# Kernel tuning notes

Hardware: AMD Instinct MI355X
Metric: run time of the kernel (lower is better)

## Reference

```python
import jax, jax.numpy as jnp
import numpy as np

NUM_HEADS = 8
NUM_LEVELS = 4
NUM_POINTS = 4


def setup_inputs() -> dict:
    key = jax.random.key(0)
    kq, kp, kv, k1, k2, k3, k4 = jax.random.split(key, 7)
    B, Q, C = 4, 4096, 256
    M, L, P = NUM_HEADS, NUM_LEVELS, NUM_POINTS
    shapes_np = np.array([[128, 128], [64, 64], [32, 32], [16, 16]], dtype=np.int32)
    sizes = shapes_np[:, 0] * shapes_np[:, 1]
    N = int(sizes.sum())  # 21760
    level_index = jnp.asarray(np.concatenate([[0], np.cumsum(sizes)[:-1]]).astype(np.int32))
    q = jax.random.normal(kq, (B, Q, C), jnp.float32)
    p = jax.random.uniform(kp, (B, Q, L, 2), jnp.float32)  # normalized ref points
    v = jax.random.normal(kv, (B, N, C), jnp.float32)
    # proj_offset bias: radial grid init from reset_parameters()
    t = np.arange(M, dtype=np.float32) * (2.0 * np.pi / M)
    grid = np.stack([np.cos(t), np.sin(t)], -1)
    grid = grid / np.abs(grid).max(-1, keepdims=True)
    grid = np.tile(grid[:, None, None, :], (1, L, P, 1)) * np.arange(1, P + 1, dtype=np.float32)[None, None, :, None]
    b_off = jnp.asarray(grid.reshape(-1))
    s = 1.0 / np.sqrt(C).astype(np.float32)
    W_off = jax.random.normal(k1, (C, M * L * P * 2), jnp.float32) * 0.01
    W_attn = jax.random.normal(k2, (C, M * L * P), jnp.float32) * s
    b_attn = jnp.zeros((M * L * P,), jnp.float32)
    W_val = jax.random.normal(k3, (C, C), jnp.float32) * s
    b_val = jnp.zeros((C,), jnp.float32)
    W_out = jax.random.normal(k4, (C, C), jnp.float32) * s
    b_out = jnp.zeros((C,), jnp.float32)
    return {"q": q, "p": p, "v": v, "shapes": jnp.asarray(shapes_np), "level_index": level_index,
            "W_off": W_off, "b_off": b_off, "W_attn": W_attn, "b_attn": b_attn,
            "W_val": W_val, "b_val": b_val, "W_out": W_out, "b_out": b_out}


def _ms_deform_attn(q, p, v, shapes, level_index, W_off, b_off, W_attn, b_attn, W_val, b_val, W_out, b_out):
    B, Q, C = q.shape
    M, L, P = NUM_HEADS, NUM_LEVELS, NUM_POINTS
    D = C // M
    N = v.shape[1]
    # value projection -> [B, M, N, D] (head-major for gather)
    v_p = (v @ W_val + b_val).reshape(B, N, M, D).transpose(0, 2, 1, 3)
    # attention weights, softmax over L*P (classic MSDeformAttn kernel contract)
    attn = jax.nn.softmax((q @ W_attn + b_attn).reshape(B, Q, M, L * P), axis=-1)
    attn = attn.reshape(B, Q, M, L, P)
    # sampling locations (P==2 reference-point branch)
    off = (q @ W_off + b_off).reshape(B, Q, M, L, P, 2)
    norm = jnp.stack([shapes[:, 1], shapes[:, 0]], -1).astype(jnp.float32)  # (W, H) per level
    loc = p[:, :, None, :, None, :] + off / norm[None, None, None, :, None, :]  # [B,Q,M,L,P,2]

    out = jnp.zeros((B, M, Q, D), jnp.float32)
    for l in range(L):
        Hf = shapes[l, 0].astype(jnp.float32)
        Wf = shapes[l, 1].astype(jnp.float32)
        Hi = shapes[l, 0]
        Wi = shapes[l, 1]
        base = level_index[l]
        # grid_sample(align_corners=False) convention: pixel = loc*size - 0.5
        x = loc[:, :, :, l, :, 0] * Wf - 0.5  # [B,Q,M,P]
        y = loc[:, :, :, l, :, 1] * Hf - 0.5
        x0 = jnp.floor(x)
        y0 = jnp.floor(y)
        lx, ly = x - x0, y - y0
        x0i = x0.astype(jnp.int32)
        y0i = y0.astype(jnp.int32)

        def corner(xi, yi, w):
            valid = (xi >= 0) & (xi < Wi) & (yi >= 0) & (yi < Hi)
            idx = base + jnp.clip(yi, 0, Hi - 1) * Wi + jnp.clip(xi, 0, Wi - 1)  # [B,Q,M,P]
            idx = idx.transpose(0, 2, 1, 3).reshape(B, M, Q * P)
            g = jnp.take_along_axis(v_p, idx[..., None], axis=2).reshape(B, M, Q, P, D)
            wv = (w * valid.astype(w.dtype)).transpose(0, 2, 1, 3)[..., None]  # [B,M,Q,P,1]
            return g * wv

        samp = (corner(x0i, y0i, (1 - lx) * (1 - ly))
                + corner(x0i + 1, y0i, lx * (1 - ly))
                + corner(x0i, y0i + 1, (1 - lx) * ly)
                + corner(x0i + 1, y0i + 1, lx * ly))  # [B,M,Q,P,D]
        a_l = attn[:, :, :, l, :].transpose(0, 2, 1, 3)  # [B,M,Q,P]
        out = out + jnp.einsum('bmqpd,bmqp->bmqd', samp, a_l)

    out = out.transpose(0, 2, 1, 3).reshape(B, Q, M * D)
    return out @ W_out + b_out


def reference(q, p, v, shapes, level_index, W_off, b_off, W_attn, b_attn, W_val, b_val, W_out, b_out):
    return _ms_deform_attn(q, p, v, shapes, level_index, W_off, b_off, W_attn, b_attn, W_val, b_val, W_out, b_out)
```

## Files before the change

kernel.cpp:

```cpp
#include <hip/hip_runtime.h>
#include <cstddef>

#define BB 4
#define QQ 4096
#define MM 8
#define NN 21760

typedef __bf16 bf16_8 __attribute__((ext_vector_type(8)));
typedef __bf16 bf16_4 __attribute__((ext_vector_type(4)));
typedef float  floatx4 __attribute__((ext_vector_type(4)));

__global__ __launch_bounds__(256) void prep_weights(
    const float* __restrict__ Wv, const float* __restrict__ Wa,
    const float* __restrict__ Wo, const float* __restrict__ Wu,
    const float* __restrict__ ba, const float* __restrict__ bo,
    __bf16* __restrict__ Wt, float* __restrict__ biasq)
{
    const int gid = blockIdx.x * 256 + threadIdx.x;
    if (gid < 65536) {
        const int n = gid >> 8, k = gid & 255;
        Wt[gid] = (__bf16)Wv[k * 256 + n];
    } else if (gid < 163840) {
        const int o = gid - 65536;
        const int n = o >> 8, k = o & 255;
        Wt[gid] = (__bf16)(n < 128 ? Wa[k * 128 + n] : Wo[k * 256 + (n - 128)]);
    } else if (gid < 229376) {
        const int o = gid - 163840;
        const int n = o >> 8, k = o & 255;
        Wt[gid] = (__bf16)Wu[k * 256 + n];
    } else if (gid < 229760) {
        const int j = gid - 229376;
        biasq[j] = (j < 128) ? ba[j] : bo[j - 128];
    }
}

template<typename AT, int NCOLS, int MODE>
__global__ __launch_bounds__(256) void gemm_bd(
    const AT* __restrict__ A,
    const __bf16* __restrict__ Wn,
    const float* __restrict__ bias,
    void* __restrict__ Cout,
    int tokens, int ldc)
{
    constexpr int NJ = NCOLS / 64;
    const int z    = blockIdx.z;
    const int row0 = blockIdx.y * 64;
    const AT* Ab = A + (size_t)z * tokens * 256;

    __shared__ __bf16 As[2][64][68];

    const int tid  = threadIdx.x;
    const int lane = tid & 63;
    const int wave = tid >> 6;
    const int quad = lane >> 4;
    const int l16  = lane & 15;
    const int wave_f = wave * (NCOLS / 4);

    floatx4 acc[NJ][4] = {};

    if (sizeof(AT) == 4) {
        const float* Af = (const float*)Ab;
        #pragma unroll
        for (int c = 0; c < 4; ++c) {
            const int cid = c * 256 + tid;
            const int r   = cid >> 4;
            const int kc  = (cid & 15) * 4;
            const float4 av = *(const float4*)(Af + (size_t)(row0 + r) * 256 + kc);
            bf16_4 w;
            w[0] = (__bf16)av.x; w[1] = (__bf16)av.y; w[2] = (__bf16)av.z; w[3] = (__bf16)av.w;
            *(bf16_4*)&As[0][r][kc] = w;
        }
    } else {
        const __bf16* Ah = (const __bf16*)Ab;
        #pragma unroll
        for (int c = 0; c < 2; ++c) {
            const int cid = c * 256 + tid;
            const int r   = cid >> 3;
            const int kc  = (cid & 7) * 8;
            *(bf16_8*)&As[0][r][kc] = *(const bf16_8*)(Ah + (size_t)(row0 + r) * 256 + kc);
        }
    }
    __syncthreads();

    for (int i = 0; i < 4; ++i) {
        const int k0  = i * 64;
        const int cur = i & 1;

        float4 a4[4]; bf16_8 a8[2];
        if (i < 3) {
            if (sizeof(AT) == 4) {
                const float* Af = (const float*)Ab;
                #pragma unroll
                for (int c = 0; c < 4; ++c) {
                    const int cid = c * 256 + tid;
                    const int r   = cid >> 4;
                    const int kc  = (cid & 15) * 4;
                    a4[c] = *(const float4*)(Af + (size_t)(row0 + r) * 256 + k0 + 64 + kc);
                }
            } else {
                const __bf16* Ah = (const __bf16*)Ab;
                #pragma unroll
                for (int c = 0; c < 2; ++c) {
                    const int cid = c * 256 + tid;
                    const int r   = cid >> 3;
                    const int kc  = (cid & 7) * 8;
                    a8[c] = *(const bf16_8*)(Ah + (size_t)(row0 + r) * 256 + k0 + 64 + kc);
                }
            }
        }

        bf16_8 wf[2][NJ];
        #pragma unroll
        for (int h = 0; h < 2; ++h)
            #pragma unroll
            for (int j = 0; j < NJ; ++j)
                wf[h][j] = *(const bf16_8*)(Wn + (size_t)(wave_f + j * 16 + l16) * 256
                                             + k0 + h * 32 + quad * 8);

        #pragma unroll
        for (int h = 0; h < 2; ++h) {
            bf16_8 af[4];
            #pragma unroll
            for (int it = 0; it < 4; ++it)
                af[it] = *(const bf16_8*)&As[cur][it * 16 + l16][h * 32 + quad * 8];
            #pragma unroll
            for (int j = 0; j < NJ; ++j)
                #pragma unroll
                for (int it = 0; it < 4; ++it)
                    acc[j][it] = __builtin_amdgcn_mfma_f32_16x16x32_bf16(wf[h][j], af[it], acc[j][it], 0, 0, 0);
        }

        if (i < 3) {
            if (sizeof(AT) == 4) {
                #pragma unroll
                for (int c = 0; c < 4; ++c) {
                    const int cid = c * 256 + tid;
                    const int r   = cid >> 4;
                    const int kc  = (cid & 15) * 4;
                    bf16_4 w;
                    w[0] = (__bf16)a4[c].x; w[1] = (__bf16)a4[c].y;
                    w[2] = (__bf16)a4[c].z; w[3] = (__bf16)a4[c].w;
                    *(bf16_4*)&As[cur ^ 1][r][kc] = w;
                }
            } else {
                #pragma unroll
                for (int c = 0; c < 2; ++c) {
                    const int cid = c * 256 + tid;
                    const int r   = cid >> 3;
                    const int kc  = (cid & 7) * 8;
                    *(bf16_8*)&As[cur ^ 1][r][kc] = a8[c];
                }
            }
            __syncthreads();
        }
    }

    #pragma unroll
    for (int j = 0; j < NJ; ++j) {
        const int n0 = wave_f + j * 16 + quad * 4;
        const float4 b4 = *(const float4*)(bias + n0);
        #pragma unroll
        for (int it = 0; it < 4; ++it) {
            const int token = row0 + it * 16 + l16;
            const float v0 = acc[j][it][0] + b4.x;
            const float v1 = acc[j][it][1] + b4.y;
            const float v2 = acc[j][it][2] + b4.z;
            const float v3 = acc[j][it][3] + b4.w;
            if (MODE == 0) {
                float4 o; o.x = v0; o.y = v1; o.z = v2; o.w = v3;
                *(float4*)((float*)Cout + ((size_t)z * tokens + token) * ldc + n0) = o;
            } else {
                const int mh = n0 >> 5, dd = n0 & 31;
                bf16_4 ob;
                ob[0] = (__bf16)v0; ob[1] = (__bf16)v1; ob[2] = (__bf16)v2; ob[3] = (__bf16)v3;
                *(bf16_4*)((__bf16*)Cout + (((size_t)z * 8 + mh) * NN + token) * 32 + dd) = ob;
            }
        }
    }
}

__device__ __forceinline__ float bflo(unsigned u) { return __uint_as_float(u << 16); }
__device__ __forceinline__ float bfhi(unsigned u) { return __uint_as_float(u & 0xffff0000u); }

__global__ __launch_bounds__(512) void sampler(
    const __bf16* __restrict__ vp,
    const float* __restrict__ gqp,
    const float* __restrict__ pref,
    __bf16* __restrict__ mid)
{
    const int t    = threadIdx.x;
    const int m    = t >> 6;
    const int lane = t & 63;
    const int s    = lane >> 2;
    const int c    = lane & 3;
    const int l    = s >> 2;
    const int bq   = blockIdx.x;
    const int b    = bq >> 12;

    const int   Hi = 128 >> l;
    const float Hf = (float)Hi;
    const int   base = (l == 0) ? 0 : (l == 1) ? 16384 : (l == 2) ? 20480 : 21504;

    const float logit = gqp[(size_t)bq * 384 + m * 16 + s];
    const float e = __expf(logit);
    float sum = e;
    #pragma unroll
    for (int k = 4; k < 64; k <<= 1) sum += __shfl_xor(sum, k, 64);
    const float a = e * __builtin_amdgcn_rcpf(sum);

    const float2 off = *(const float2*)(gqp + (size_t)bq * 384 + 128 + (m * 16 + s) * 2);
    const float2 pr  = *(const float2*)(pref + (size_t)bq * 8 + l * 2);

    const float x = fmaf(pr.x, Hf, off.x - 0.5f);
    const float y = fmaf(pr.y, Hf, off.y - 0.5f);
    const float x0f = floorf(x), y0f = floorf(y);
    const float lx = x - x0f, ly = y - y0f;
    const int x0 = (int)x0f, y0 = (int)y0f;
    const int cx0 = min(max(x0, 0), Hi - 1), cx1 = min(max(x0 + 1, 0), Hi - 1);
    const int cy0 = min(max(y0, 0), Hi - 1), cy1 = min(max(y0 + 1, 0), Hi - 1);
    const bool vx0 = (x0 >= 0) && (x0 < Hi), vx1 = (x0 + 1 >= 0) && (x0 + 1 < Hi);
    const bool vy0 = (y0 >= 0) && (y0 < Hi), vy1 = (y0 + 1 >= 0) && (y0 + 1 < Hi);
    const float w00 = a * (1.f - lx) * (1.f - ly) * ((vx0 && vy0) ? 1.f : 0.f);
    const float w10 = a * lx * (1.f - ly) * ((vx1 && vy0) ? 1.f : 0.f);
    const float w01 = a * (1.f - lx) * ly * ((vx0 && vy1) ? 1.f : 0.f);
    const float w11 = a * lx * ly * ((vx1 && vy1) ? 1.f : 0.f);

    const __bf16* vbase = vp + ((size_t)b * 8 + m) * NN * 32;
    const uint4 u00 = *((const uint4*)(vbase + (size_t)(base + cy0 * Hi + cx0) * 32) + c);
    const uint4 u10 = *((const uint4*)(vbase + (size_t)(base + cy0 * Hi + cx1) * 32) + c);
    const uint4 u01 = *((const uint4*)(vbase + (size_t)(base + cy1 * Hi + cx0) * 32) + c);
    const uint4 u11 = *((const uint4*)(vbase + (size_t)(base + cy1 * Hi + cx1) * 32) + c);

    float f[8];
    f[0] = w00*bflo(u00.x) + w10*bflo(u10.x) + w01*bflo(u01.x) + w11*bflo(u11.x);
    f[1] = w00*bfhi(u00.x) + w10*bfhi(u10.x) + w01*bfhi(u01.x) + w11*bfhi(u11.x);
    f[2] = w00*bflo(u00.y) + w10*bflo(u10.y) + w01*bflo(u01.y) + w11*bflo(u11.y);
    f[3] = w00*bfhi(u00.y) + w10*bfhi(u10.y) + w01*bfhi(u01.y) + w11*bfhi(u11.y);
    f[4] = w00*bflo(u00.z) + w10*bflo(u10.z) + w01*bflo(u01.z) + w11*bflo(u11.z);
    f[5] = w00*bfhi(u00.z) + w10*bfhi(u10.z) + w01*bfhi(u01.z) + w11*bfhi(u11.z);
    f[6] = w00*bflo(u00.w) + w10*bflo(u10.w) + w01*bflo(u01.w) + w11*bflo(u11.w);
    f[7] = w00*bfhi(u00.w) + w10*bfhi(u10.w) + w01*bfhi(u01.w) + w11*bfhi(u11.w);

    const int b2 = (lane >> 2) & 1, b3 = (lane >> 3) & 1, b4i = (lane >> 4) & 1;
    #pragma unroll
    for (int j = 0; j < 4; ++j) {
        const float sel  = b2 ? f[j] : f[j + 4];
        const float recv = __shfl_xor(sel, 4, 64);
        f[j] = (b2 ? f[j + 4] : f[j]) + recv;
    }
    #pragma unroll
    for (int j = 0; j < 2; ++j) {
        const float sel  = b3 ? f[j] : f[j + 2];
        const float recv = __shfl_xor(sel, 8, 64);
        f[j] = (b3 ? f[j + 2] : f[j]) + recv;
    }
    {
        const float sel  = b4i ? f[0] : f[1];
        const float recv = __shfl_xor(sel, 16, 64);
        f[0] = (b4i ? f[1] : f[0]) + recv;
    }
    f[0] += __shfl_xor(f[0], 32, 64);

    if (!(lane & 32)) {
        const int chan = (c << 3) | (b2 << 2) | (b3 << 1) | b4i;
        mid[(size_t)bq * 256 + m * 32 + chan] = (__bf16)f[0];
    }
}

extern "C" void kernel_launch(void* const* d_in, const int* in_sizes, int n_in,
                              void* d_out, int out_size, void* d_ws, size_t ws_size,
                              hipStream_t stream) {
    const float* q      = (const float*)d_in[0];
    const float* p      = (const float*)d_in[1];
    const float* v      = (const float*)d_in[2];
    const float* W_off  = (const float*)d_in[5];
    const float* b_off  = (const float*)d_in[6];
    const float* W_attn = (const float*)d_in[7];
    const float* b_attn = (const float*)d_in[8];
    const float* W_val  = (const float*)d_in[9];
    const float* b_val  = (const float*)d_in[10];
    const float* W_out  = (const float*)d_in[11];
    const float* b_out  = (const float*)d_in[12];
    float* out = (float*)d_out;

    float*  gqp   = (float*)d_ws;
    float*  biasq = gqp + (size_t)16384 * 384;
    __bf16* mid   = (__bf16*)(biasq + 384);
    __bf16* vpb   = mid + (size_t)16384 * 256;
    __bf16* Wt    = vpb + (size_t)BB * 8 * NN * 32;
    __bf16* Wt_val  = Wt;
    __bf16* Wt_attn = Wt + 65536;
    __bf16* Wt_off  = Wt + 65536 + 32768;
    __bf16* Wt_out  = Wt + 163840;

    prep_weights<<<898, 256, 0, stream>>>(W_val, W_attn, W_off, W_out, b_attn, b_off, Wt, biasq);

    {
        dim3 grid(1, NN / 64, BB);
        gemm_bd<float, 256, 1><<<grid, 256, 0, stream>>>(v, Wt_val, b_val, vpb, NN, 0);
    }
    {
        dim3 grid(1, (BB * QQ) / 64, 1);
        gemm_bd<float, 128, 0><<<grid, 256, 0, stream>>>(q, Wt_attn, biasq, gqp, BB * QQ, 384);
    }
    {
        dim3 grid(1, (BB * QQ) / 64, 1);
        gemm_bd<float, 256, 0><<<grid, 256, 0, stream>>>(q, Wt_off, biasq + 128, gqp + 128, BB * QQ, 384);
    }
    sampler<<<BB * QQ, 512, 0, stream>>>(vpb, gqp, p, mid);
    {
        dim3 grid(1, (BB * QQ) / 64, 1);
        gemm_bd<__bf16, 256, 0><<<grid, 256, 0, stream>>>(mid, Wt_out, b_out, out, BB * QQ, 256);
    }
}
```

Before: 263.3 us.

## Keep GEMM weights register-resident across multiple token tiles with full-K swizzled LDS

Replaces the 256-thread K-chunked GEMM with a 512-thread kernel. Each wave loads its whole weight slice (all of K) into registers once and reuses it across several 64-token tiles (4 tiles for the value projection). The A tile is staged as full-K rows in XOR-swizzled LDS, and the next tile is prefetched in two halves overlapped with the MFMA loops. This cuts repeated global weight reads and LDS bank conflicts, at the cost of heavy register pressure (up to 8x4 bf16x8 weight fragments plus accumulators) and fewer blocks for the value GEMM.

```diff
diff --git a/kernel.cpp b/kernel.cpp
--- a/kernel.cpp
+++ b/kernel.cpp
@@ -34,148 +34,231 @@
     }
 }
 
-template<typename AT, int NCOLS, int MODE>
-__global__ __launch_bounds__(256) void gemm_bd(
+template<typename AT, int NCOLS, int MODE, int TILES>
+__global__ __launch_bounds__(512) void gemm_ws(
     const AT* __restrict__ A,
     const __bf16* __restrict__ Wn,
     const float* __restrict__ bias,
     void* __restrict__ Cout,
     int tokens, int ldc)
 {
-    constexpr int NJ = NCOLS / 64;
-    const int z    = blockIdx.z;
-    const int row0 = blockIdx.y * 64;
+    constexpr int F  = NCOLS / 8;
+    constexpr int NJ = F / 16;
+
+    const int z = blockIdx.z;
     const AT* Ab = A + (size_t)z * tokens * 256;
 
-    __shared__ __bf16 As[2][64][68];
+    __shared__ __bf16 As[2][64][256];
 
     const int tid  = threadIdx.x;
     const int lane = tid & 63;
     const int wave = tid >> 6;
     const int quad = lane >> 4;
     const int l16  = lane & 15;
-    const int wave_f = wave * (NCOLS / 4);
-
-    floatx4 acc[NJ][4] = {};
-
-    if (sizeof(AT) == 4) {
-        const float* Af = (const float*)Ab;
+    const int wave_f = wave * F;
+
+    bf16_8 wf[8][NJ];
+    #pragma unroll
+    for (int kk = 0; kk < 8; ++kk)
         #pragma unroll
-        for (int c = 0; c < 4; ++c) {
-            const int cid = c * 256 + tid;
-            const int r   = cid >> 4;
-            const int kc  = (cid & 15) * 4;
-            const float4 av = *(const float4*)(Af + (size_t)(row0 + r) * 256 + kc);
-            bf16_4 w;
-            w[0] = (__bf16)av.x; w[1] = (__bf16)av.y; w[2] = (__bf16)av.z; w[3] = (__bf16)av.w;
-            *(bf16_4*)&As[0][r][kc] = w;
-        }
-    } else {
-        const __bf16* Ah = (const __bf16*)Ab;
-        #pragma unroll
-        for (int c = 0; c < 2; ++c) {
-            const int cid = c * 256 + tid;
-            const int r   = cid >> 3;
-            const int kc  = (cid & 7) * 8;
-            *(bf16_8*)&As[0][r][kc] = *(const bf16_8*)(Ah + (size_t)(row0 + r) * 256 + kc);
-        }
-    }
-    __syncthreads();
-
-    for (int i = 0; i < 4; ++i) {
-        const int k0  = i * 64;
-        const int cur = i & 1;
+        for (int j = 0; j < NJ; ++j)
+            wf[kk][j] = *(const bf16_8*)(Wn + (size_t)(wave_f + j * 16 + l16) * 256
+                                          + kk * 32 + quad * 8);
+
+    const int tile0 = blockIdx.y * TILES;
+
+
+    {
+        const int token0 = tile0 * 64;
+        if (sizeof(AT) == 4) {
+            const float* Af = (const float*)Ab;
+            #pragma unroll
+            for (int h = 0; h < 2; ++h) {
+                #pragma unroll
+                for (int c = 0; c < 4; ++c) {
+                    const int cid = c * 512 + tid;
+                    const int r   = cid >> 5;
+                    const int kc  = (cid & 31) * 4;
+                    const int k   = h * 128 + kc;
+                    const float4 av = *(const float4*)(Af + (size_t)(token0 + r) * 256 + k);
+                    bf16_4 w;
+                    w[0] = (__bf16)av.x; w[1] = (__bf16)av.y;
+                    w[2] = (__bf16)av.z; w[3] = (__bf16)av.w;
+                    const int col = ((((k >> 3) ^ (r & 7)) << 3) | (k & 7));
+                    *(bf16_4*)&As[0][r][col] = w;
+                }
+            }
+        } else {
+            const __bf16* Ah = (const __bf16*)Ab;
+            #pragma unroll
+            for (int h = 0; h < 2; ++h) {
+                #pragma unroll
+                for (int c = 0; c < 2; ++c) {
+                    const int cid = c * 512 + tid;
+                    const int r   = cid >> 4;
+                    const int kc  = (cid & 15) * 8;
+                    const int k   = h * 128 + kc;
+                    const bf16_8 av = *(const bf16_8*)(Ah + (size_t)(token0 + r) * 256 + k);
+                    const int col = (((k >> 3) ^ (r & 7)) << 3);
+                    *(bf16_8*)&As[0][r][col] = av;
+                }
+            }
+        }
+        __syncthreads();
+    }
+
+    #pragma unroll
+    for (int t = 0; t < TILES; ++t) {
+        const int cur    = t & 1;
+        const int token0 = (tile0 + t) * 64;
+        const bool more  = (t + 1 < TILES);
+        const int ntok0  = token0 + 64;
+
+        floatx4 acc[NJ][4] = {};
 
         float4 a4[4]; bf16_8 a8[2];
-        if (i < 3) {
+        if (more) {
             if (sizeof(AT) == 4) {
                 const float* Af = (const float*)Ab;
                 #pragma unroll
                 for (int c = 0; c < 4; ++c) {
-                    const int cid = c * 256 + tid;
-                    const int r   = cid >> 4;
-                    const int kc  = (cid & 15) * 4;
-                    a4[c] = *(const float4*)(Af + (size_t)(row0 + r) * 256 + k0 + 64 + kc);
+                    const int cid = c * 512 + tid;
+                    const int r   = cid >> 5;
+                    const int kc  = (cid & 31) * 4;
+                    a4[c] = *(const float4*)(Af + (size_t)(ntok0 + r) * 256 + kc);
                 }
             } else {
                 const __bf16* Ah = (const __bf16*)Ab;
                 #pragma unroll
                 for (int c = 0; c < 2; ++c) {
-                    const int cid = c * 256 + tid;
-                    const int r   = cid >> 3;
-                    const int kc  = (cid & 7) * 8;
-                    a8[c] = *(const bf16_8*)(Ah + (size_t)(row0 + r) * 256 + k0 + 64 + kc);
-                }
-            }
-        }
-
-        bf16_8 wf[2][NJ];
+                    const int cid = c * 512 + tid;
+                    const int r   = cid >> 4;
+                    const int kc  = (cid & 15) * 8;
+                    a8[c] = *(const bf16_8*)(Ah + (size_t)(ntok0 + r) * 256 + kc);
+                }
+            }
+        }
+
         #pragma unroll
-        for (int h = 0; h < 2; ++h)
+        for (int kk = 0; kk < 4; ++kk) {
+            bf16_8 af[4];
+            #pragma unroll
+            for (int it = 0; it < 4; ++it)
+                af[it] = *(const bf16_8*)&As[cur][it * 16 + l16]
+                                           [(((kk * 4 + quad) ^ (l16 & 7)) << 3)];
             #pragma unroll
             for (int j = 0; j < NJ; ++j)
-                wf[h][j] = *(const bf16_8*)(Wn + (size_t)(wave_f + j * 16 + l16) * 256
-                                             + k0 + h * 32 + quad * 8);
-
-        #pragma unroll
-        for (int h = 0; h < 2; ++h) {
-            bf16_8 af[4];
-            #pragma unroll
-            for (int it = 0; it < 4; ++it)
-                af[it] = *(const bf16_8*)&As[cur][it * 16 + l16][h * 32 + quad * 8];
-            #pragma unroll
-            for (int j = 0; j < NJ; ++j)
                 #pragma unroll
                 for (int it = 0; it < 4; ++it)
-                    acc[j][it] = __builtin_amdgcn_mfma_f32_16x16x32_bf16(wf[h][j], af[it], acc[j][it], 0, 0, 0);
-        }
-
-        if (i < 3) {
+                    acc[j][it] = __builtin_amdgcn_mfma_f32_16x16x32_bf16(wf[kk][j], af[it], acc[j][it], 0, 0, 0);
+        }
+
+        if (more) {
             if (sizeof(AT) == 4) {
-                #pragma unroll
-                for (int c = 0; c < 4; ++c) {
-                    const int cid = c * 256 + tid;
-                    const int r   = cid >> 4;
-                    const int kc  = (cid & 15) * 4;
+                const float* Af = (const float*)Ab;
+                #pragma unroll
+                for (int c = 0; c < 4; ++c) {
+                    const int cid = c * 512 + tid;
+                    const int r   = cid >> 5;
+                    const int kc  = (cid & 31) * 4;
                     bf16_4 w;
                     w[0] = (__bf16)a4[c].x; w[1] = (__bf16)a4[c].y;
                     w[2] = (__bf16)a4[c].z; w[3] = (__bf16)a4[c].w;
-                    *(bf16_4*)&As[cur ^ 1][r][kc] = w;
+                    const int col = ((((kc >> 3) ^ (r & 7)) << 3) | (kc & 7));
+                    *(bf16_4*)&As[cur ^ 1][r][col] = w;
+                }
+                #pragma unroll
+                for (int c = 0; c < 4; ++c) {
+                    const int cid = c * 512 + tid;
+                    const int r   = cid >> 5;
+                    const int kc  = (cid & 31) * 4;
+                    a4[c] = *(const float4*)(Af + (size_t)(ntok0 + r) * 256 + 128 + kc);
                 }
             } else {
-                #pragma unroll
-                for (int c = 0; c < 2; ++c) {
-                    const int cid = c * 256 + tid;
-                    const int r   = cid >> 3;
-                    const int kc  = (cid & 7) * 8;
-                    *(bf16_8*)&As[cur ^ 1][r][kc] = a8[c];
-                }
-            }
-            __syncthreads();
-        }
-    }
-
-    #pragma unroll
-    for (int j = 0; j < NJ; ++j) {
-        const int n0 = wave_f + j * 16 + quad * 4;
-        const float4 b4 = *(const float4*)(bias + n0);
+                const __bf16* Ah = (const __bf16*)Ab;
+                #pragma unroll
+                for (int c = 0; c < 2; ++c) {
+                    const int cid = c * 512 + tid;
+                    const int r   = cid >> 4;
+                    const int kc  = (cid & 15) * 8;
+                    const int col = (((kc >> 3) ^ (r & 7)) << 3);
+                    *(bf16_8*)&As[cur ^ 1][r][col] = a8[c];
+                }
+                #pragma unroll
+                for (int c = 0; c < 2; ++c) {
+                    const int cid = c * 512 + tid;
+                    const int r   = cid >> 4;
+                    const int kc  = (cid & 15) * 8;
+                    a8[c] = *(const bf16_8*)(Ah + (size_t)(ntok0 + r) * 256 + 128 + kc);
+                }
+            }
+        }
+
         #pragma unroll
-        for (int it = 0; it < 4; ++it) {
-            const int token = row0 + it * 16 + l16;
-            const float v0 = acc[j][it][0] + b4.x;
-            const float v1 = acc[j][it][1] + b4.y;
-            const float v2 = acc[j][it][2] + b4.z;
-            const float v3 = acc[j][it][3] + b4.w;
-            if (MODE == 0) {
-                float4 o; o.x = v0; o.y = v1; o.z = v2; o.w = v3;
-                *(float4*)((float*)Cout + ((size_t)z * tokens + token) * ldc + n0) = o;
+        for (int kk = 4; kk < 8; ++kk) {
+            bf16_8 af[4];
+            #pragma unroll
+            for (int it = 0; it < 4; ++it)
+                af[it] = *(const bf16_8*)&As[cur][it * 16 + l16]
+                                           [(((kk * 4 + quad) ^ (l16 & 7)) << 3)];
+            #pragma unroll
+            for (int j = 0; j < NJ; ++j)
+                #pragma unroll
+                for (int it = 0; it < 4; ++it)
+                    acc[j][it] = __builtin_amdgcn_mfma_f32_16x16x32_bf16(wf[kk][j], af[it], acc[j][it], 0, 0, 0);
+        }
+
+        if (more) {
+            if (sizeof(AT) == 4) {
+                #pragma unroll
+                for (int c = 0; c < 4; ++c) {
+                    const int cid = c * 512 + tid;
+                    const int r   = cid >> 5;
+                    const int kc  = (cid & 31) * 4;
+                    const int k   = 128 + kc;
+                    bf16_4 w;
+                    w[0] = (__bf16)a4[c].x; w[1] = (__bf16)a4[c].y;
+                    w[2] = (__bf16)a4[c].z; w[3] = (__bf16)a4[c].w;
+                    const int col = ((((k >> 3) ^ (r & 7)) << 3) | (k & 7));
+                    *(bf16_4*)&As[cur ^ 1][r][col] = w;
+                }
             } else {
-                const int mh = n0 >> 5, dd = n0 & 31;
-                bf16_4 ob;
-                ob[0] = (__bf16)v0; ob[1] = (__bf16)v1; ob[2] = (__bf16)v2; ob[3] = (__bf16)v3;
-                *(bf16_4*)((__bf16*)Cout + (((size_t)z * 8 + mh) * NN + token) * 32 + dd) = ob;
-            }
-        }
+                #pragma unroll
+                for (int c = 0; c < 2; ++c) {
+                    const int cid = c * 512 + tid;
+                    const int r   = cid >> 4;
+                    const int kc  = (cid & 15) * 8;
+                    const int k   = 128 + kc;
+                    const int col = (((k >> 3) ^ (r & 7)) << 3);
+                    *(bf16_8*)&As[cur ^ 1][r][col] = a8[c];
+                }
+            }
+        }
+
+        #pragma unroll
+        for (int j = 0; j < NJ; ++j) {
+            const int n0 = wave_f + j * 16 + quad * 4;
+            const float4 b4 = *(const float4*)(bias + n0);
+            #pragma unroll
+            for (int it = 0; it < 4; ++it) {
+                const int token = token0 + it * 16 + l16;
+                const float v0 = acc[j][it][0] + b4.x;
+                const float v1 = acc[j][it][1] + b4.y;
+                const float v2 = acc[j][it][2] + b4.z;
+                const float v3 = acc[j][it][3] + b4.w;
+                if (MODE == 0) {
+                    float4 o; o.x = v0; o.y = v1; o.z = v2; o.w = v3;
+                    *(float4*)((float*)Cout + ((size_t)z * tokens + token) * ldc + n0) = o;
+                } else {
+                    const int mh = n0 >> 5, dd = n0 & 31;
+                    bf16_4 ob;
+                    ob[0] = (__bf16)v0; ob[1] = (__bf16)v1; ob[2] = (__bf16)v2; ob[3] = (__bf16)v3;
+                    *(bf16_4*)((__bf16*)Cout + (((size_t)z * 8 + mh) * NN + token) * 32 + dd) = ob;
+                }
+            }
+        }
+
+        if (more) __syncthreads();
     }
 }
 
@@ -296,20 +379,20 @@
     prep_weights<<<898, 256, 0, stream>>>(W_val, W_attn, W_off, W_out, b_attn, b_off, Wt, biasq);
 
     {
-        dim3 grid(1, NN / 64, BB);
-        gemm_bd<float, 256, 1><<<grid, 256, 0, stream>>>(v, Wt_val, b_val, vpb, NN, 0);
-    }
-    {
-        dim3 grid(1, (BB * QQ) / 64, 1);
-        gemm_bd<float, 128, 0><<<grid, 256, 0, stream>>>(q, Wt_attn, biasq, gqp, BB * QQ, 384);
-    }
-    {
-        dim3 grid(1, (BB * QQ) / 64, 1);
-        gemm_bd<float, 256, 0><<<grid, 256, 0, stream>>>(q, Wt_off, biasq + 128, gqp + 128, BB * QQ, 384);
+        dim3 grid(1, 340 / 4, BB);
+        gemm_ws<float, 256, 1, 4><<<grid, 512, 0, stream>>>(v, Wt_val, b_val, vpb, NN, 0);
+    }
+    {
+        dim3 grid(1, 256, 1);
+        gemm_ws<float, 128, 0, 1><<<grid, 512, 0, stream>>>(q, Wt_attn, biasq, gqp, BB * QQ, 384);
+    }
+    {
+        dim3 grid(1, 256, 1);
+        gemm_ws<float, 256, 0, 1><<<grid, 512, 0, stream>>>(q, Wt_off, biasq + 128, gqp + 128, BB * QQ, 384);
     }
     sampler<<<BB * QQ, 512, 0, stream>>>(vpb, gqp, p, mid);
     {
-        dim3 grid(1, (BB * QQ) / 64, 1);
-        gemm_bd<__bf16, 256, 0><<<grid, 256, 0, stream>>>(mid, Wt_out, b_out, out, BB * QQ, 256);
+        dim3 grid(1, 256, 1);
+        gemm_ws<__bf16, 256, 0, 1><<<grid, 512, 0, stream>>>(mid, Wt_out, b_out, out, BB * QQ, 256);
     }
 }
```

Result: faster. 252.1 us (-4.2%).
